# Kernel tuning notes

Measured on AMD Instinct MI355X. Metric: run time of the kernel, lower is better.

Reference implementation:

```python
import jax, jax.numpy as jnp
import numpy as np

RADIUS = 2
SIGMA_SPATIAL = 2.5
SIGMA_RANGE_FACTOR = 0.5


def setup_inputs() -> dict:
    key = jax.random.key(0)
    k1, k2 = jax.random.split(key)
    source = jax.random.normal(k1, (4, 64, 64, 64), dtype=jnp.float32)
    guidance = jax.random.uniform(k2, (4, 3, 256, 256), dtype=jnp.float32)
    return {"source": source, "guidance": guidance}


def _jbu(source, guidance):
    # source: [B, C, h, w] low-res features; guidance: [B, Cg, H, W] high-res image
    B, C, h, w = source.shape
    _, Cg, H, W = guidance.shape
    s = H // h  # integer upsampling factor
    r = RADIUS

    # per-batch range sigma from guidance std (torch.std is unbiased -> ddof=1)
    sigma_range = SIGMA_RANGE_FACTOR * jnp.std(guidance, axis=(1, 2, 3), ddof=1)  # [B]
    inv_2sr2 = 1.0 / (2.0 * sigma_range * sigma_range)  # [B]
    inv_2ss2 = 1.0 / (2.0 * SIGMA_SPATIAL * SIGMA_SPATIAL)

    # guidance sampled at low-res cell centers: [B, Cg, h, w]
    off = s // 2
    g_low = guidance[:, :, off::s, off::s]

    # low-res center index for every hi-res pixel
    yc = jnp.arange(H) // s  # [H]
    xc = jnp.arange(W) // s  # [W]

    num = jnp.zeros((B, C, H, W), dtype=source.dtype)
    den = jnp.zeros((B, 1, H, W), dtype=source.dtype)

    # fixed small (2r+1)^2 = 25 window taps; unrolled loop, each tap is a
    # clamped gather + fused weight compute + accumulate (no huge intermediates)
    for dy in range(-r, r + 1):
        yi = jnp.clip(yc + dy, 0, h - 1)  # [H]
        for dx in range(-r, r + 1):
            xi = jnp.clip(xc + dx, 0, w - 1)  # [W]
            src_g = source[:, :, yi[:, None], xi[None, :]]  # [B, C, H, W]
            g_g = g_low[:, :, yi[:, None], xi[None, :]]      # [B, Cg, H, W]
            diff2 = jnp.sum((guidance - g_g) ** 2, axis=1)   # [B, H, W]
            w_range = jnp.exp(-diff2 * inv_2sr2[:, None, None])
            w_spatial = np.exp(-(dy * dy + dx * dx) * 1.0) ** 0.0  # placeholder removed below
            w_spatial = jnp.exp(jnp.asarray(-(dy * dy + dx * dx) * inv_2ss2, dtype=source.dtype))
            wgt = (w_spatial * w_range)[:, None]  # [B, 1, H, W]
            num = num + src_g * wgt
            den = den + wgt

    return num / (den + 1e-8)


def reference(source, guidance):
    return _jbu(source, guidance)
```

## Files before the change

### kernel.cpp

```cpp
#include <hip/hip_runtime.h>

#define B_  4
#define C_  64
#define H_  256
#define W_  256
#define h_  64
#define w_  64
#define L2SW2 (-0.46166241f)
#define L2SW1 (-0.11541560f)

__global__ void jbu_stats(const float* __restrict__ g, double* __restrict__ stats) {
    int b     = blockIdx.x >> 5;
    int slice = blockIdx.x & 31;
    const float4* p = (const float4*)(g + (size_t)b * 3 * H_ * W_) + (size_t)slice * 1536;
    double s = 0.0, s2 = 0.0;
    for (int i = threadIdx.x; i < 1536; i += 256) {
        float4 v = p[i];
        s  += (double)v.x + (double)v.y + (double)v.z + (double)v.w;
        s2 += (double)v.x * v.x + (double)v.y * v.y
            + (double)v.z * v.z + (double)v.w * v.w;
    }
    for (int off = 32; off > 0; off >>= 1) {
        s  += __shfl_down(s,  off);
        s2 += __shfl_down(s2, off);
    }
    __shared__ double ls[8];
    int wid  = threadIdx.x >> 6;
    int lane = threadIdx.x & 63;
    if (lane == 0) { ls[wid] = s; ls[4 + wid] = s2; }
    __syncthreads();
    if (threadIdx.x == 0) {
        stats[blockIdx.x]       = ls[0] + ls[1] + ls[2] + ls[3];
        stats[128 + blockIdx.x] = ls[4] + ls[5] + ls[6] + ls[7];
    }
}

__global__ __launch_bounds__(256, 4)
void jbu_mega16(const float* __restrict__ src, const float* __restrict__ guid,
                const double* __restrict__ stats, float* __restrict__ out) {
    __shared__ __align__(16) float sS[5 * 64 * 20];
    __shared__ __align__(16) float sG[5 * 64 * 4];

    int cg  = blockIdx.x & 3;
    int y4  = (blockIdx.x >> 2) & 63;
    int b   = blockIdx.x >> 8;
    int tid = threadIdx.x;

    const float* sb = src + ((size_t)b * C_ + cg * 16) * h_ * w_;
    #pragma unroll
    for (int it = 0; it < 20; ++it) {
        int k   = tid + it * 256;
        int xx  = k & 63;
        int cr  = k >> 6;
        int row = cr >> 4;
        int cc  = cr & 15;
        int u   = y4 + row - 2;
        int yy  = u < 0 ? 0 : (u > h_ - 1 ? h_ - 1 : u);
        sS[(row * 64 + xx) * 20 + cc] = sb[((size_t)cc * h_ + yy) * w_ + xx];
    }
    {
        int k = tid;
        #pragma unroll
        for (int it = 0; it < 4; ++it) {
            if (k < 960) {
                int xx  = k & 63;
                int cr  = k >> 6;
                int row = cr / 3;
                int c   = cr - row * 3;
                int u   = y4 + row - 2;
                int yy  = u < 0 ? 0 : (u > h_ - 1 ? h_ - 1 : u);
                sG[(row * 64 + xx) * 4 + c] =
                    guid[(((size_t)b * 3 + c) * H_ + (yy * 4 + 2)) * W_ + (xx * 4 + 2)];
            }
            k += 256;
        }
    }

    double S = 0.0, S2 = 0.0;
    for (int i = 0; i < 32; ++i) {
        S  += stats[b * 32 + i];
        S2 += stats[128 + b * 32 + i];
    }
    const double n = 3.0 * H_ * W_;
    double var = (S2 - S * S / n) / (n - 1.0);
    float invrl2 = (float)(2.0 / var) * 1.44269504f;

    __syncthreads();

    int x  = tid;
    int y0 = y4 * 4;

    float gp[4][3];
    #pragma unroll
    for (int c = 0; c < 3; ++c)
        #pragma unroll
        for (int p = 0; p < 4; ++p)
            gp[p][c] = guid[(((size_t)b * 3 + c) * H_ + (y0 + p)) * W_ + x];

    int xb = x >> 2;
    int xi[5];
    #pragma unroll
    for (int d = 0; d < 5; ++d) {
        int v = xb + d - 2;
        xi[d] = v < 0 ? 0 : (v > w_ - 1 ? w_ - 1 : v);
    }

    const float l2sw[5] = {L2SW2, L2SW1, 0.0f, L2SW1, L2SW2};

    float acc[4][16];
    float den[4];
    #pragma unroll
    for (int p = 0; p < 4; ++p) {
        den[p] = 0.0f;
        #pragma unroll
        for (int c = 0; c < 16; ++c) acc[p][c] = 0.0f;
    }

    #pragma unroll
    for (int dy = 0; dy < 5; ++dy) {
        float l2y = l2sw[dy];
        int   rb  = dy * 64;
        #pragma unroll
        for (int dx = 0; dx < 5; ++dx) {
            int xx = xi[dx];
            float4 gl = *(const float4*)&sG[(rb + xx) * 4];
            float l2xy = l2y + l2sw[dx];
            float wgt[4];
            #pragma unroll
            for (int p = 0; p < 4; ++p) {
                float d0 = gp[p][0] - gl.x;
                float d1 = gp[p][1] - gl.y;
                float d2 = gp[p][2] - gl.z;
                float diff2 = fmaf(d2, d2, fmaf(d1, d1, d0 * d0));
                float wv = __builtin_amdgcn_exp2f(fmaf(diff2, -invrl2, l2xy));
                wgt[p] = wv;
                den[p] += wv;
            }
            const float* sP = &sS[(rb + xx) * 20];
            #pragma unroll
            for (int q = 0; q < 4; ++q) {
                float4 sv = *(const float4*)(sP + q * 4);
                #pragma unroll
                for (int p = 0; p < 4; ++p) {
                    acc[p][q * 4 + 0] = fmaf(wgt[p], sv.x, acc[p][q * 4 + 0]);
                    acc[p][q * 4 + 1] = fmaf(wgt[p], sv.y, acc[p][q * 4 + 1]);
                    acc[p][q * 4 + 2] = fmaf(wgt[p], sv.z, acc[p][q * 4 + 2]);
                    acc[p][q * 4 + 3] = fmaf(wgt[p], sv.w, acc[p][q * 4 + 3]);
                }
            }
        }
    }

    float* ob = out + ((size_t)b * C_ + cg * 16) * H_ * W_;
    #pragma unroll
    for (int p = 0; p < 4; ++p) {
        float r = 1.0f / (den[p] + 1e-8f);
        int row = (y0 + p) * W_ + x;
        #pragma unroll
        for (int c = 0; c < 16; ++c) {
            ob[(size_t)c * H_ * W_ + row] = acc[p][c] * r;
        }
    }
}

extern "C" void kernel_launch(void* const* d_in, const int* in_sizes, int n_in,
                              void* d_out, int out_size, void* d_ws, size_t ws_size,
                              hipStream_t stream) {
    const float* src  = (const float*)d_in[0];
    const float* guid = (const float*)d_in[1];
    float* out = (float*)d_out;

    double* stats = (double*)d_ws;

    jbu_stats<<<128, 256, 0, stream>>>(guid, stats);
    jbu_mega16<<<B_ * 64 * 4, 256, 0, stream>>>(src, guid, stats, out);
}
```

Baseline: 97.73 us.

## Expand range-weight squared distance algebraically and vectorize shared-memory staging loads

The squared guidance difference inside the exponent is expanded into a dot product plus precomputed per-pixel and per-tap norm terms. The tap norm is stored in the fourth slot of each shared guidance entry, which cuts the per-tap arithmetic in the inner loop. The source tile staging is also changed to load four channels per thread and write them as one float4 to shared memory, and the guidance staging now fetches all three channels per thread. The expanded form can lose floating-point precision through cancellation when the two guidance values are close, which slightly changes the weights.

```diff
diff --git a/kernel.cpp b/kernel.cpp
--- a/kernel.cpp
+++ b/kernel.cpp
@@ -46,36 +46,6 @@
     int b   = blockIdx.x >> 8;
     int tid = threadIdx.x;
 
-    const float* sb = src + ((size_t)b * C_ + cg * 16) * h_ * w_;
-    #pragma unroll
-    for (int it = 0; it < 20; ++it) {
-        int k   = tid + it * 256;
-        int xx  = k & 63;
-        int cr  = k >> 6;
-        int row = cr >> 4;
-        int cc  = cr & 15;
-        int u   = y4 + row - 2;
-        int yy  = u < 0 ? 0 : (u > h_ - 1 ? h_ - 1 : u);
-        sS[(row * 64 + xx) * 20 + cc] = sb[((size_t)cc * h_ + yy) * w_ + xx];
-    }
-    {
-        int k = tid;
-        #pragma unroll
-        for (int it = 0; it < 4; ++it) {
-            if (k < 960) {
-                int xx  = k & 63;
-                int cr  = k >> 6;
-                int row = cr / 3;
-                int c   = cr - row * 3;
-                int u   = y4 + row - 2;
-                int yy  = u < 0 ? 0 : (u > h_ - 1 ? h_ - 1 : u);
-                sG[(row * 64 + xx) * 4 + c] =
-                    guid[(((size_t)b * 3 + c) * H_ + (yy * 4 + 2)) * W_ + (xx * 4 + 2)];
-            }
-            k += 256;
-        }
-    }
-
     double S = 0.0, S2 = 0.0;
     for (int i = 0; i < 32; ++i) {
         S  += stats[b * 32 + i];
@@ -85,17 +55,62 @@
     double var = (S2 - S * S / n) / (n - 1.0);
     float invrl2 = (float)(2.0 / var) * 1.44269504f;
 
+    int yi[5];
+    #pragma unroll
+    for (int d = 0; d < 5; ++d) {
+        int u = y4 + d - 2;
+        yi[d] = u < 0 ? 0 : (u > h_ - 1 ? h_ - 1 : u);
+    }
+
+    const float* sb = src + ((size_t)b * C_ + cg * 16) * h_ * w_;
+    {
+        int xx0 = tid & 63;
+        int j4  = ((tid >> 6) & 3) * 4;
+        #pragma unroll
+        for (int it = 0; it < 5; ++it) {
+            int yy = yi[it];
+            float4 v;
+            v.x = sb[((size_t)(j4 + 0) * h_ + yy) * w_ + xx0];
+            v.y = sb[((size_t)(j4 + 1) * h_ + yy) * w_ + xx0];
+            v.z = sb[((size_t)(j4 + 2) * h_ + yy) * w_ + xx0];
+            v.w = sb[((size_t)(j4 + 3) * h_ + yy) * w_ + xx0];
+            *(float4*)&sS[(it * 64 + xx0) * 20 + j4] = v;
+        }
+    }
+    for (int k = tid; k < 320; k += 256) {
+        int xx  = k & 63;
+        int row = k >> 6;
+        int u   = y4 + row - 2;
+        int yy  = u < 0 ? 0 : (u > h_ - 1 ? h_ - 1 : u);
+        const float* gbase = guid + (size_t)b * 3 * H_ * W_
+                           + (size_t)(yy * 4 + 2) * W_ + (xx * 4 + 2);
+        float gx = gbase[0];
+        float gy = gbase[H_ * W_];
+        float gz = gbase[2 * H_ * W_];
+        float ss = fmaf(gz, gz, fmaf(gy, gy, gx * gx));
+        float4 e = make_float4(gx, gy, gz, -invrl2 * ss);
+        *(float4*)&sG[(row * 64 + xx) * 4] = e;
+    }
+
     __syncthreads();
 
     int x  = tid;
     int y0 = y4 * 4;
 
     float gp[4][3];
+    float A[4];
     #pragma unroll
     for (int c = 0; c < 3; ++c)
         #pragma unroll
         for (int p = 0; p < 4; ++p)
             gp[p][c] = guid[(((size_t)b * 3 + c) * H_ + (y0 + p)) * W_ + x];
+    float t2 = 2.0f * invrl2;
+    #pragma unroll
+    for (int p = 0; p < 4; ++p) {
+        float ss = fmaf(gp[p][2], gp[p][2], fmaf(gp[p][1], gp[p][1], gp[p][0] * gp[p][0]));
+        A[p] = -invrl2 * ss;
+        gp[p][0] *= t2; gp[p][1] *= t2; gp[p][2] *= t2;
+    }
 
     int xb = x >> 2;
     int xi[5];
@@ -124,15 +139,13 @@
         for (int dx = 0; dx < 5; ++dx) {
             int xx = xi[dx];
             float4 gl = *(const float4*)&sG[(rb + xx) * 4];
-            float l2xy = l2y + l2sw[dx];
+            float ct = gl.w + (l2y + l2sw[dx]);
             float wgt[4];
             #pragma unroll
             for (int p = 0; p < 4; ++p) {
-                float d0 = gp[p][0] - gl.x;
-                float d1 = gp[p][1] - gl.y;
-                float d2 = gp[p][2] - gl.z;
-                float diff2 = fmaf(d2, d2, fmaf(d1, d1, d0 * d0));
-                float wv = __builtin_amdgcn_exp2f(fmaf(diff2, -invrl2, l2xy));
+                float m = fmaf(gp[p][2], gl.z,
+                          fmaf(gp[p][1], gl.y, gp[p][0] * gl.x));
+                float wv = __builtin_amdgcn_exp2f(m + ct + A[p]);
                 wgt[p] = wv;
                 den[p] += wv;
             }
```

Result: no change. 96.59 us (-1.2%).
